# Kernel optimization log

Hardware: AMD Instinct MI355X
Metric: run time of the kernel (lower is better)

The kernel has to match this reference:

```python
import jax, jax.numpy as jnp
import numpy as np

IN_CH, OUT_CH, K, DIL = 64, 128, 3, 8

def setup_inputs() -> dict:
    key = jax.random.key(0)
    k1, k2, k3 = jax.random.split(key, 3)
    x = jax.random.normal(k1, (16, IN_CH, 128, 128), dtype=jnp.float32)
    # xavier_normal-like init for W
    fan_in, fan_out = IN_CH * K * K, OUT_CH * K * K
    std = (2.0 / (fan_in + fan_out)) ** 0.5
    W = jax.random.normal(k2, (OUT_CH, IN_CH, K, K), dtype=jnp.float32) * std
    b = jax.random.normal(k3, (OUT_CH,), dtype=jnp.float32)
    return {"x": x, "W": W, "b": b}

def reference(x, W, b):
    pad = DIL * (K // 2)  # circular halo so output spatial size == input
    xp = jnp.pad(x, ((0, 0), (0, 0), (pad, pad), (pad, pad)), mode="wrap")
    y = jax.lax.conv_general_dilated(
        xp, W,
        window_strides=(1, 1),
        padding="VALID",
        rhs_dilation=(DIL, DIL),
        dimension_numbers=("NCHW", "OIHW", "NCHW"),
    )
    return y + b[None, :, None, None]
```

## Files before the change

### kernel.cpp

```cpp
#include <hip/hip_runtime.h>

#define IN_CH 64
#define OUT_CH 128
#define HW 128
#define KTAPS 9
#define ROWB 16384

typedef __bf16 bf16x8 __attribute__((ext_vector_type(8)));
typedef float f32x16 __attribute__((ext_vector_type(16)));
typedef float f32x4 __attribute__((ext_vector_type(4)));

__device__ __forceinline__ unsigned f2bf(float f) {
    unsigned u = __builtin_bit_cast(unsigned, f);
    return (u + 0x7FFFu + ((u >> 16) & 1u)) >> 16;
}

__device__ __forceinline__ int swz(int r) { return ((r ^ (r >> 3)) & 7) << 4; }

__global__ void wprep_kernel(const float* __restrict__ W, unsigned short* __restrict__ Wl) {
    int i = blockIdx.x * blockDim.x + threadIdx.x;
    if (i >= OUT_CH * IN_CH * KTAPS) return;
    int p  = i / 36864;
    int r  = i % 36864;
    int t  = r >> 12;
    int r2 = r & 4095;
    int m  = r2 >> 11;
    int ks = (r2 >> 9) & 3;
    int l  = (r2 >> 3) & 63;
    int e  = r2 & 7;
    int oc = p * 64 + m * 32 + (l & 31);
    int ic = ks * 16 + (l >> 5) * 8 + e;
    int kh = t / 3, kw = t % 3;
    Wl[i] = (unsigned short)f2bf(W[((oc * IN_CH + ic) * 3 + kh) * 3 + kw]);
}

__global__ __launch_bounds__(256, 3) void conv_kernel_f(
    const float* __restrict__ x, const unsigned short* __restrict__ Wl,
    const float* __restrict__ bias, float* __restrict__ y)
{
    __shared__ __align__(16) unsigned char xsB[3 * ROWB];

    int bid = blockIdx.x;
    int sb  = (bid & 7) * 256 + (bid >> 3);
    int n = sb >> 7, h = sb & 127;
    int tid = threadIdx.x;
    int wid = tid >> 6, lane = tid & 63;
    int wr = wid >> 1, wc = wid & 1;
    int l31 = lane & 31, lhi = lane >> 5;

    const bf16x8* Ab = reinterpret_cast<const bf16x8*>(Wl) + wr * (9 * 512) + lane;

    bf16x8 aBuf[2][8];
    #pragma unroll
    for (int j = 0; j < 8; ++j) aBuf[0][j] = Ab[j * 64];

    #pragma unroll
    for (int it = 0; it < 3; ++it) {
        int q   = it * 256 + tid;
        int w4  = q & 31;
        int ic8 = (q >> 5) & 7;
        int kh  = q >> 8;
        int srow = (h + kh * 8 + 120) & 127;
        const float* xp = x + (((n * IN_CH + ic8 * 8) * HW + srow) * HW + w4 * 4);
        f32x4 v[8];
        #pragma unroll
        for (int j = 0; j < 8; ++j)
            v[j] = *reinterpret_cast<const f32x4*>(xp + j * (HW * HW));
        #pragma unroll
        for (int j2 = 0; j2 < 4; ++j2) {
            int w = w4 * 4 + j2;
            uint4 pk;
            pk.x = f2bf(v[0][j2]) | (f2bf(v[1][j2]) << 16);
            pk.y = f2bf(v[2][j2]) | (f2bf(v[3][j2]) << 16);
            pk.z = f2bf(v[4][j2]) | (f2bf(v[5][j2]) << 16);
            pk.w = f2bf(v[6][j2]) | (f2bf(v[7][j2]) << 16);
            *reinterpret_cast<uint4*>(xsB + kh * ROWB + ((w * 128 + ic8 * 16) ^ swz(w))) = pk;
        }
    }
    __syncthreads();

    f32x16 acc[2][2];
    #pragma unroll
    for (int a = 0; a < 2; ++a)
        #pragma unroll
        for (int bq = 0; bq < 2; ++bq)
            #pragma unroll
            for (int r = 0; r < 16; ++r) acc[a][bq][r] = 0.0f;

    #pragma unroll
    for (int t = 0; t < 9; ++t) {
        if (t < 8) {
            #pragma unroll
            for (int j = 0; j < 8; ++j)
                aBuf[(t + 1) & 1][j] = Ab[(t + 1) * 512 + j * 64];
        }
        int kh = t / 3, kw = t % 3;
        int xc0 = (wc * 64 + l31 + 8 * kw - 8) & 127;
        int xc1 = (xc0 + 32) & 127;
        int b0base = kh * ROWB + xc0 * 128 + lhi * 16, s0 = swz(xc0);
        int b1base = kh * ROWB + xc1 * 128 + lhi * 16, s1 = swz(xc1);
        #pragma unroll
        for (int ks = 0; ks < 4; ++ks) {
            bf16x8 a0 = aBuf[t & 1][ks];
            bf16x8 a1 = aBuf[t & 1][4 + ks];
            bf16x8 b0 = *reinterpret_cast<const bf16x8*>(xsB + ((b0base + ks * 32) ^ s0));
            bf16x8 b1 = *reinterpret_cast<const bf16x8*>(xsB + ((b1base + ks * 32) ^ s1));
            acc[0][0] = __builtin_amdgcn_mfma_f32_32x32x16_bf16(a0, b0, acc[0][0], 0, 0, 0);
            acc[0][1] = __builtin_amdgcn_mfma_f32_32x32x16_bf16(a0, b1, acc[0][1], 0, 0, 0);
            acc[1][0] = __builtin_amdgcn_mfma_f32_32x32x16_bf16(a1, b0, acc[1][0], 0, 0, 0);
            acc[1][1] = __builtin_amdgcn_mfma_f32_32x32x16_bf16(a1, b1, acc[1][1], 0, 0, 0);
        }
    }

    int outbase = (n * OUT_CH) * HW * HW + h * HW;
    #pragma unroll
    for (int mi = 0; mi < 2; ++mi) {
        #pragma unroll
        for (int ni = 0; ni < 2; ++ni) {
            int wcol = wc * 64 + ni * 32 + l31;
            #pragma unroll
            for (int reg = 0; reg < 16; ++reg) {
                int oc = wr * 64 + mi * 32 + (reg & 3) + 8 * (reg >> 2) + 4 * lhi;
                y[outbase + oc * HW * HW + wcol] = acc[mi][ni][reg] + bias[oc];
            }
        }
    }
}

extern "C" void kernel_launch(void* const* d_in, const int* in_sizes, int n_in,
                              void* d_out, int out_size, void* d_ws, size_t ws_size,
                              hipStream_t stream) {
    const float* x = (const float*)d_in[0];
    const float* W = (const float*)d_in[1];
    const float* b = (const float*)d_in[2];
    float* y = (float*)d_out;

    unsigned short* Wl = (unsigned short*)d_ws;

    hipLaunchKernelGGL(wprep_kernel, dim3((OUT_CH * IN_CH * KTAPS + 255) / 256), dim3(256), 0, stream, W, Wl);
    hipLaunchKernelGGL(conv_kernel_f, dim3(16 * HW), dim3(256), 0, stream, x, Wl, b, y);
}
```

Baseline: 68.25 us.

## Double-buffer LDS B-fragments, raise MFMA priority, use nontemporal output stores

Prefetches the next tap's B fragments from LDS into a register double buffer, alongside the existing A prefetch, so LDS latency overlaps the current tap's MFMAs. Wraps the MFMA block in s_setprio to favour matrix issue, and writes the output with nontemporal stores so the large fp32 result does not pollute cache. Launch bounds drop from 3 to 2 blocks per CU to make room for the extra registers, which may reduce occupancy and latency hiding of the global loads.

```diff
diff --git a/kernel.cpp b/kernel.cpp
--- a/kernel.cpp
+++ b/kernel.cpp
@@ -34,7 +34,7 @@
     Wl[i] = (unsigned short)f2bf(W[((oc * IN_CH + ic) * 3 + kh) * 3 + kw]);
 }
 
-__global__ __launch_bounds__(256, 3) void conv_kernel_f(
+__global__ __launch_bounds__(256, 2) void conv_kernel_f(
     const float* __restrict__ x, const unsigned short* __restrict__ Wl,
     const float* __restrict__ bias, float* __restrict__ y)
 {
@@ -87,29 +87,50 @@
             #pragma unroll
             for (int r = 0; r < 16; ++r) acc[a][bq][r] = 0.0f;
 
+    bf16x8 bBuf[2][8];
+    {
+        int xc0 = (wc * 64 + l31 + 8 * 0 - 8) & 127;
+        int xc1 = (xc0 + 32) & 127;
+        int b0base = 0 * ROWB + xc0 * 128 + lhi * 16, s0 = swz(xc0);
+        int b1base = 0 * ROWB + xc1 * 128 + lhi * 16, s1 = swz(xc1);
+        #pragma unroll
+        for (int ks = 0; ks < 4; ++ks) {
+            bBuf[0][ks]     = *reinterpret_cast<const bf16x8*>(xsB + ((b0base + ks * 32) ^ s0));
+            bBuf[0][4 + ks] = *reinterpret_cast<const bf16x8*>(xsB + ((b1base + ks * 32) ^ s1));
+        }
+    }
+
     #pragma unroll
     for (int t = 0; t < 9; ++t) {
         if (t < 8) {
+            int tn = t + 1;
             #pragma unroll
             for (int j = 0; j < 8; ++j)
-                aBuf[(t + 1) & 1][j] = Ab[(t + 1) * 512 + j * 64];
+                aBuf[tn & 1][j] = Ab[tn * 512 + j * 64];
+            int kh = tn / 3, kw = tn % 3;
+            int xc0 = (wc * 64 + l31 + 8 * kw - 8) & 127;
+            int xc1 = (xc0 + 32) & 127;
+            int b0base = kh * ROWB + xc0 * 128 + lhi * 16, s0 = swz(xc0);
+            int b1base = kh * ROWB + xc1 * 128 + lhi * 16, s1 = swz(xc1);
+            #pragma unroll
+            for (int ks = 0; ks < 4; ++ks) {
+                bBuf[tn & 1][ks]     = *reinterpret_cast<const bf16x8*>(xsB + ((b0base + ks * 32) ^ s0));
+                bBuf[tn & 1][4 + ks] = *reinterpret_cast<const bf16x8*>(xsB + ((b1base + ks * 32) ^ s1));
+            }
         }
-        int kh = t / 3, kw = t % 3;
-        int xc0 = (wc * 64 + l31 + 8 * kw - 8) & 127;
-        int xc1 = (xc0 + 32) & 127;
-        int b0base = kh * ROWB + xc0 * 128 + lhi * 16, s0 = swz(xc0);
-        int b1base = kh * ROWB + xc1 * 128 + lhi * 16, s1 = swz(xc1);
+        __builtin_amdgcn_s_setprio(1);
         #pragma unroll
         for (int ks = 0; ks < 4; ++ks) {
             bf16x8 a0 = aBuf[t & 1][ks];
             bf16x8 a1 = aBuf[t & 1][4 + ks];
-            bf16x8 b0 = *reinterpret_cast<const bf16x8*>(xsB + ((b0base + ks * 32) ^ s0));
-            bf16x8 b1 = *reinterpret_cast<const bf16x8*>(xsB + ((b1base + ks * 32) ^ s1));
+            bf16x8 b0 = bBuf[t & 1][ks];
+            bf16x8 b1 = bBuf[t & 1][4 + ks];
             acc[0][0] = __builtin_amdgcn_mfma_f32_32x32x16_bf16(a0, b0, acc[0][0], 0, 0, 0);
             acc[0][1] = __builtin_amdgcn_mfma_f32_32x32x16_bf16(a0, b1, acc[0][1], 0, 0, 0);
             acc[1][0] = __builtin_amdgcn_mfma_f32_32x32x16_bf16(a1, b0, acc[1][0], 0, 0, 0);
             acc[1][1] = __builtin_amdgcn_mfma_f32_32x32x16_bf16(a1, b1, acc[1][1], 0, 0, 0);
         }
+        __builtin_amdgcn_s_setprio(0);
     }
 
     int outbase = (n * OUT_CH) * HW * HW + h * HW;
@@ -121,7 +142,8 @@
             #pragma unroll
             for (int reg = 0; reg < 16; ++reg) {
                 int oc = wr * 64 + mi * 32 + (reg & 3) + 8 * (reg >> 2) + 4 * lhi;
-                y[outbase + oc * HW * HW + wcol] = acc[mi][ni][reg] + bias[oc];
+                __builtin_nontemporal_store(acc[mi][ni][reg] + bias[oc],
+                                            &y[outbase + oc * HW * HW + wcol]);
             }
         }
     }
```

After: 68.45 us. About the same (+0.3%).

## Split conv block work across 8 waves with smaller per-wave output tiles

Applied to the files above, without the earlier changes.

Doubles the block to 512 threads so each wave computes a 32x64 output tile instead of 64x64, halving accumulators and weight registers per wave. The weight double-buffer prefetch is dropped in favour of loading the current tap's A fragments just before use. The aim is more waves in flight to hide LDS and global latency. The cost is that each B fragment read from LDS is now reused across half as many MFMAs, and the weight loads are no longer prefetched.

```diff
diff --git a/kernel.cpp b/kernel.cpp
--- a/kernel.cpp
+++ b/kernel.cpp
@@ -34,7 +34,7 @@
     Wl[i] = (unsigned short)f2bf(W[((oc * IN_CH + ic) * 3 + kh) * 3 + kw]);
 }
 
-__global__ __launch_bounds__(256, 3) void conv_kernel_f(
+__global__ __launch_bounds__(512, 6) void conv_kernel_f(
     const float* __restrict__ x, const unsigned short* __restrict__ Wl,
     const float* __restrict__ bias, float* __restrict__ y)
 {
@@ -45,18 +45,8 @@
     int n = sb >> 7, h = sb & 127;
     int tid = threadIdx.x;
     int wid = tid >> 6, lane = tid & 63;
-    int wr = wid >> 1, wc = wid & 1;
-    int l31 = lane & 31, lhi = lane >> 5;
 
-    const bf16x8* Ab = reinterpret_cast<const bf16x8*>(Wl) + wr * (9 * 512) + lane;
-
-    bf16x8 aBuf[2][8];
-    #pragma unroll
-    for (int j = 0; j < 8; ++j) aBuf[0][j] = Ab[j * 64];
-
-    #pragma unroll
-    for (int it = 0; it < 3; ++it) {
-        int q   = it * 256 + tid;
+    for (int q = tid; q < 768; q += 512) {
         int w4  = q & 31;
         int ic8 = (q >> 5) & 7;
         int kh  = q >> 8;
@@ -79,21 +69,25 @@
     }
     __syncthreads();
 
-    f32x16 acc[2][2];
+    int wr = wid >> 1, wc = wid & 1;
+    int l31 = lane & 31, lhi = lane >> 5;
+    int p = wr >> 1, m = wr & 1;
+
+    const bf16x8* Ab = reinterpret_cast<const bf16x8*>(Wl)
+                     + p * (9 * 512) + m * 256 + lane;
+
+    f32x16 acc[2];
     #pragma unroll
-    for (int a = 0; a < 2; ++a)
+    for (int bq = 0; bq < 2; ++bq)
         #pragma unroll
-        for (int bq = 0; bq < 2; ++bq)
-            #pragma unroll
-            for (int r = 0; r < 16; ++r) acc[a][bq][r] = 0.0f;
+        for (int r = 0; r < 16; ++r) acc[bq][r] = 0.0f;
 
     #pragma unroll
     for (int t = 0; t < 9; ++t) {
-        if (t < 8) {
-            #pragma unroll
-            for (int j = 0; j < 8; ++j)
-                aBuf[(t + 1) & 1][j] = Ab[(t + 1) * 512 + j * 64];
-        }
+        bf16x8 aCur[4];
+        #pragma unroll
+        for (int ks = 0; ks < 4; ++ks) aCur[ks] = Ab[t * 512 + ks * 64];
+
         int kh = t / 3, kw = t % 3;
         int xc0 = (wc * 64 + l31 + 8 * kw - 8) & 127;
         int xc1 = (xc0 + 32) & 127;
@@ -101,28 +95,21 @@
         int b1base = kh * ROWB + xc1 * 128 + lhi * 16, s1 = swz(xc1);
         #pragma unroll
         for (int ks = 0; ks < 4; ++ks) {
-            bf16x8 a0 = aBuf[t & 1][ks];
-            bf16x8 a1 = aBuf[t & 1][4 + ks];
             bf16x8 b0 = *reinterpret_cast<const bf16x8*>(xsB + ((b0base + ks * 32) ^ s0));
             bf16x8 b1 = *reinterpret_cast<const bf16x8*>(xsB + ((b1base + ks * 32) ^ s1));
-            acc[0][0] = __builtin_amdgcn_mfma_f32_32x32x16_bf16(a0, b0, acc[0][0], 0, 0, 0);
-            acc[0][1] = __builtin_amdgcn_mfma_f32_32x32x16_bf16(a0, b1, acc[0][1], 0, 0, 0);
-            acc[1][0] = __builtin_amdgcn_mfma_f32_32x32x16_bf16(a1, b0, acc[1][0], 0, 0, 0);
-            acc[1][1] = __builtin_amdgcn_mfma_f32_32x32x16_bf16(a1, b1, acc[1][1], 0, 0, 0);
+            acc[0] = __builtin_amdgcn_mfma_f32_32x32x16_bf16(aCur[ks], b0, acc[0], 0, 0, 0);
+            acc[1] = __builtin_amdgcn_mfma_f32_32x32x16_bf16(aCur[ks], b1, acc[1], 0, 0, 0);
         }
     }
 
     int outbase = (n * OUT_CH) * HW * HW + h * HW;
     #pragma unroll
-    for (int mi = 0; mi < 2; ++mi) {
+    for (int bq = 0; bq < 2; ++bq) {
+        int wcol = wc * 64 + bq * 32 + l31;
         #pragma unroll
-        for (int ni = 0; ni < 2; ++ni) {
-            int wcol = wc * 64 + ni * 32 + l31;
-            #pragma unroll
-            for (int reg = 0; reg < 16; ++reg) {
-                int oc = wr * 64 + mi * 32 + (reg & 3) + 8 * (reg >> 2) + 4 * lhi;
-                y[outbase + oc * HW * HW + wcol] = acc[mi][ni][reg] + bias[oc];
-            }
+        for (int reg = 0; reg < 16; ++reg) {
+            int oc = wr * 32 + (reg & 3) + 8 * (reg >> 2) + 4 * lhi;
+            y[outbase + oc * HW * HW + wcol] = acc[bq][reg] + bias[oc];
         }
     }
 }
@@ -138,5 +125,5 @@
     unsigned short* Wl = (unsigned short*)d_ws;
 
     hipLaunchKernelGGL(wprep_kernel, dim3((OUT_CH * IN_CH * KTAPS + 255) / 256), dim3(256), 0, stream, W, Wl);
-    hipLaunchKernelGGL(conv_kernel_f, dim3(16 * HW), dim3(256), 0, stream, x, Wl, b, y);
+    hipLaunchKernelGGL(conv_kernel_f, dim3(16 * HW), dim3(512), 0, stream, x, Wl, b, y);
 }
```

After: 64.02 us. 6.2% less time.
